# Performance work log

Hardware: AMD Instinct MI355X
Metric: run time of the kernel (lower is better)

## Reference

```python
import jax, jax.numpy as jnp
import numpy as np

MAX_DEPTH = 11  # node positions < 2**11 = 2048


def setup_inputs() -> dict:
    key = jax.random.key(0)
    k1, k2, k3, k4, k5 = jax.random.split(key, 5)
    B, S, dim = 4, 1024, 64
    token_types = jax.random.randint(k1, (B, S), 0, 5).astype(jnp.int32)
    # token_values in [-1, 2]: -1 marks out-of-scope for scope tokens;
    # bop uses tv+1 (0..3), nop uses tv+5 (4..7) -- all in-range for the 11-row table
    token_values = (jax.random.randint(k2, (B, S), 0, 4) - 1).astype(jnp.int32)
    node_positions = jax.random.randint(k3, (B, S), 0, 2048).astype(jnp.int32)
    embed_table = jax.random.normal(k4, (11, dim), dtype=jnp.float32)
    # mirrors torch.rand(2,dim,dim).softmax(-1).cumsum(-1) init
    primitives_raw = jnp.cumsum(
        jax.nn.softmax(jax.random.uniform(k5, (2, dim, dim), dtype=jnp.float32), axis=-1),
        axis=-1)
    return {
        "token_types": token_types,
        "token_values": token_values,
        "node_positions": node_positions,
        "embed_table": embed_table,
        "primitives_raw": primitives_raw,
    }


def _forward(token_types, token_values, node_positions, embed_table, primitives_raw):
    dim = embed_table.shape[1]
    B, S = token_types.shape

    # primitives = expm(P - P^H) for each of the 2 generators
    herm = primitives_raw - jnp.swapaxes(primitives_raw, -1, -2)
    prims = jax.vmap(jax.scipy.linalg.expm)(herm)  # [2, dim, dim]

    # --- positional encodings via binary-path matrix products ---
    # path(pos) applies prims[pos%2], then prims[(pos//2)%2], ... until pos==1.
    # Equivalent to the original's per-unique-position masked-linear loop,
    # evaluated per token (== positional_encodings[inverse]).
    maps = jnp.broadcast_to(jnp.eye(dim, dtype=embed_table.dtype), (B, S, dim, dim))
    pos = node_positions
    for _ in range(MAX_DEPTH):
        active = pos > 1
        bit = (pos & 1).astype(jnp.int32)
        step_p = prims[bit]  # [B, S, dim, dim] gather of the per-step generator
        # linear(maps, prim) == maps @ prim.T, applied rowwise to each map matrix
        stepped = jnp.einsum('bsij,bskj->bsik', maps, step_p)
        maps = jnp.where(active[..., None, None], stepped, maps)
        pos = pos >> 1

    # --- content embeddings via masked gathers ---
    tt, tv = token_types, token_values
    sos = tt == 0
    bop = tt == 1
    nop = tt == 2
    scope = tt == 3
    oos = scope & (tv == -1)
    db = tt == 4
    idx = jnp.where(sos, 0,
          jnp.where(bop, tv + 1,
          jnp.where(nop, tv + 5,
          jnp.where(db, 8,
          jnp.where(oos, 10, 0)))))
    valid = sos | bop | nop | db | oos  # in-scope scope tokens stay zero
    content = jnp.where(valid[..., None], embed_table[idx], jnp.zeros((), embed_table.dtype))
    return content, maps


def reference(token_types, token_values, node_positions, embed_table, primitives_raw):
    return _forward(token_types, token_values, node_positions, embed_table, primitives_raw)
```

## Files before the change

kernel.cpp:

```cpp
#include <hip/hip_runtime.h>
#include <hip/hip_bf16.h>
#include <stdint.h>

typedef __attribute__((ext_vector_type(4))) float fx4;
typedef __attribute__((ext_vector_type(16))) float fx16;
typedef __attribute__((ext_vector_type(8))) short bx8;
typedef unsigned short u16;
typedef unsigned int u32;

#define LDW 72
#define PL (64 * LDW)
#define MAGIC 0x9E3779B9u


__device__ __forceinline__ u16 f2bf(float x) {
    u32 u = __float_as_uint(x);
    return (u16)((u + 0x7FFFu + ((u >> 16) & 1u)) >> 16);
}
__device__ __forceinline__ float bf2f(u16 h) { return __uint_as_float(((u32)h) << 16); }

__device__ __forceinline__ bx8 ld32(const u16* p, int band, int kc, int l) {
    return *(const bx8*)(p + (band * 32 + (l & 31)) * LDW + kc * 16 + (l >> 5) * 8);
}

__device__ __forceinline__ void mmS(const u16* z1h, const u16* z1l,
                                    const u16* z2h, const u16* z2l,
                                    int ti, int tj, int l, fx16& acc) {
    fx16 chh, chl, clh;
#pragma unroll
    for (int i = 0; i < 16; ++i) { chh[i] = 0.f; chl[i] = 0.f; clh[i] = 0.f; }
#pragma unroll
    for (int kc = 0; kc < 4; ++kc) {
        bx8 ah = ld32(z1h, ti, kc, l), al = ld32(z1l, ti, kc, l);
        bx8 bh = ld32(z2h, tj, kc, l), bl = ld32(z2l, tj, kc, l);
        chh = __builtin_amdgcn_mfma_f32_32x32x16_bf16(ah, bh, chh, 0, 0, 0);
        chl = __builtin_amdgcn_mfma_f32_32x32x16_bf16(ah, bl, chl, 0, 0, 0);
        clh = __builtin_amdgcn_mfma_f32_32x32x16_bf16(al, bh, clh, 0, 0, 0);
    }
#pragma unroll
    for (int i = 0; i < 16; ++i) acc[i] = chh[i] + (chl[i] + clh[i]);
}

__device__ __forceinline__ void mmD(const u16* z1h, const u16* z1l,
                                    const u16* z2h, const u16* z2l,
                                    int ti, int tj, int l, fx16& a1, fx16& a2) {
    fx16 c1a, c1b, c1c, c2a, c2b, c2c;
#pragma unroll
    for (int i = 0; i < 16; ++i) {
        c1a[i] = 0.f; c1b[i] = 0.f; c1c[i] = 0.f;
        c2a[i] = 0.f; c2b[i] = 0.f; c2c[i] = 0.f;
    }
#pragma unroll
    for (int kc = 0; kc < 4; ++kc) {
        bx8 ah = ld32(z1h, ti, kc, l), al = ld32(z1l, ti, kc, l);
        bx8 bh = ld32(z2h, tj, kc, l), bl = ld32(z2l, tj, kc, l);
        c1a = __builtin_amdgcn_mfma_f32_32x32x16_bf16(ah, bh, c1a, 0, 0, 0);
        c1b = __builtin_amdgcn_mfma_f32_32x32x16_bf16(ah, bl, c1b, 0, 0, 0);
        c1c = __builtin_amdgcn_mfma_f32_32x32x16_bf16(al, bh, c1c, 0, 0, 0);
        c2a = __builtin_amdgcn_mfma_f32_32x32x16_bf16(bh, ah, c2a, 0, 0, 0);
        c2b = __builtin_amdgcn_mfma_f32_32x32x16_bf16(bh, al, c2b, 0, 0, 0);
        c2c = __builtin_amdgcn_mfma_f32_32x32x16_bf16(bl, ah, c2c, 0, 0, 0);
    }
#pragma unroll
    for (int i = 0; i < 16; ++i) {
        a1[i] = c1a[i] + (c1b[i] + c1c[i]);
        a2[i] = c2a[i] + (c2b[i] + c2c[i]);
    }
}

__device__ __forceinline__ void stP(u16* hi, u16* lo, int TI, int TJ, int l, const fx16& a) {
    const int Ar = TJ * 32 + (l & 31);
    const int c0 = TI * 32 + 4 * (l >> 5);
#pragma unroll
    for (int q = 0; q < 4; ++q) {
        union { u16 u[4]; uint2 v; } H, L;
#pragma unroll
        for (int r = 0; r < 4; ++r) {
            float v = a[4 * q + r];
            u32 u = __float_as_uint(v);
            H.u[r] = (u16)(u >> 16);
            L.u[r] = f2bf(v - __uint_as_float(u & 0xFFFF0000u));
        }
        *(uint2*)(hi + Ar * LDW + c0 + q * 8) = H.v;
        *(uint2*)(lo + Ar * LDW + c0 + q * 8) = L.v;
    }
}

__device__ __forceinline__ void stG(u16* T, int TI, int TJ, int l, const fx16& a) {
    const int Ar = TJ * 32 + (l & 31);
    const int c0 = TI * 32 + 4 * (l >> 5);
#pragma unroll
    for (int q = 0; q < 4; ++q) {
        union { u16 u[4]; uint2 v; } pk;
#pragma unroll
        for (int r = 0; r < 4; ++r) pk.u[r] = f2bf(a[4 * q + r]);
        *(uint2*)(T + Ar * 64 + c0 + q * 8) = pk.v;
    }
}

__device__ __forceinline__ void epiT32(fx16& a, const float* Mf,
                                       int TI, int TJ, int l, float qa, float qb) {
    const int gc = TJ * 32 + (l & 31);
    const int r0 = TI * 32 + 4 * (l >> 5);
#pragma unroll
    for (int q = 0; q < 4; ++q)
#pragma unroll
        for (int r = 0; r < 4; ++r) {
            const int gr = r0 + q * 8 + r;
            float m = Mf[gc * 65 + gr];
            a[4 * q + r] += qb * m + (gr == gc ? qa : 0.f);
        }
}
__device__ __forceinline__ void epiN32(fx16& a, const float* Mf,
                                       int TI, int TJ, int l, float qa, float qb) {
    const int gc = TJ * 32 + (l & 31);
    const int r0 = TI * 32 + 4 * (l >> 5);
#pragma unroll
    for (int q = 0; q < 4; ++q)
#pragma unroll
        for (int r = 0; r < 4; ++r) {
            const int gr = r0 + q * 8 + r;
            float m = Mf[gr * 65 + gc];
            a[4 * q + r] += qb * m + (gr == gc ? qa : 0.f);
        }
}

__global__ __launch_bounds__(256) void tables_kernel(const float* __restrict__ praw,
                                                     u16* __restrict__ wsP,
                                                     u16* __restrict__ rm_bf,
                                                     u16* __restrict__ cm_bf,
                                                     u32* __restrict__ flags)
{
    __shared__ u16 S[8 * PL];
    __shared__ float Mf[64 * 65];
    const int p = blockIdx.x, tid = threadIdx.x;
    const int w = tid >> 6, l = tid & 63;
    const int ti = w & 1, tj = w >> 1;

    if (p < 2) {
        const int g = p;
        const float* P = praw + g * 4096;
        u16* p0h = S;            u16* p0l = S + PL;
        u16* p1h = S + 2 * PL;   u16* p1l = S + 3 * PL;
        u16* p2h = S + 4 * PL;   u16* p2l = S + 5 * PL;
        u16* p3h = S + 6 * PL;   u16* p3l = S + 7 * PL;

        for (int s = tid; s < 4096; s += 256) {
            const int r = s >> 6, c = s & 63;
            const float m = (P[r * 64 + c] - P[c * 64 + r]) * 0.03125f;
            Mf[r * 65 + c] = m;
            u32 um = __float_as_uint(m);
            float lof = m - __uint_as_float(um & 0xFFFF0000u);
            u16 hh = (u16)(um >> 16), ll = f2bf(lof);
            p0h[r * LDW + c] = hh;  p0l[r * LDW + c] = ll;
            p1h[c * LDW + r] = hh;  p1l[c * LDW + r] = ll;
        }
        __syncthreads();

        fx16 acc, a1, a2;

        mmS(p1h, p1l, p0h, p0l, ti, tj, l, acc);
        stP(p2h, p2l, ti, tj, l, acc);
        {
            const float C8 = 2.48015873015873e-5f, C9 = 2.75573192239859e-6f;
            for (int s = tid; s < 4096; s += 256) {
                const int r = s >> 6, c = s & 63;
                float v = C9 * Mf[r * 65 + c] + (r == c ? C8 : 0.f);
                u32 u = __float_as_uint(v);
                p3h[r * LDW + c] = (u16)(u >> 16);
                p3l[r * LDW + c] = f2bf(v - __uint_as_float(u & 0xFFFF0000u));
            }
        }
        __syncthreads();

        mmS(p2h, p2l, p3h, p3l, ti, tj, l, acc);
        epiT32(acc, Mf, ti, tj, l, 1.388888888888889e-3f, 1.984126984126984e-4f);
        stP(p0h, p0l, ti, tj, l, acc);
        __syncthreads();
        mmS(p2h, p2l, p0h, p0l, ti, tj, l, acc);
        epiT32(acc, Mf, ti, tj, l, 4.166666666666667e-2f, 8.333333333333333e-3f);
        stP(p3h, p3l, ti, tj, l, acc);
        __syncthreads();
        mmS(p2h, p2l, p3h, p3l, ti, tj, l, acc);
        epiT32(acc, Mf, ti, tj, l, 0.5f, 1.666666666666667e-1f);
        stP(p0h, p0l, ti, tj, l, acc);
        __syncthreads();
        mmD(p2h, p2l, p0h, p0l, ti, tj, l, a1, a2);
        epiT32(a1, Mf, ti, tj, l, 1.f, 1.f);
        epiN32(a2, Mf, tj, ti, l, 1.f, 1.f);
        stP(p3h, p3l, ti, tj, l, a1);
        stP(p1h, p1l, tj, ti, l, a2);
        __syncthreads();

        u16 *Ych = p1h, *Ycl = p1l, *Xch = p3h, *Xcl = p3l;
        u16 *Ynh = p2h, *Ynl = p2l, *Xnh = p0h, *Xnl = p0l;
#pragma unroll 1
        for (int s5 = 0; s5 < 5; ++s5) {
            mmD(Ych, Ycl, Xch, Xcl, ti, tj, l, a1, a2);
            stP(Xnh, Xnl, ti, tj, l, a1);
            stP(Ynh, Ynl, tj, ti, l, a2);
            __syncthreads();
            u16* t;
            t = Xch; Xch = Xnh; Xnh = t;   t = Xcl; Xcl = Xnl; Xnl = t;
            t = Ych; Ych = Ynh; Ynh = t;   t = Ycl; Ycl = Ynl; Ynl = t;
        }

        for (int s8 = tid; s8 < 512; s8 += 256) {
            const int base = s8 * 8, r = base >> 6, c = base & 63;
            u16* dst = wsP + g * 16384;
            *(uint4*)(dst + base)         = *(const uint4*)(Ych + r * LDW + c);
            *(uint4*)(dst + 4096 + base)  = *(const uint4*)(Ycl + r * LDW + c);
            *(uint4*)(dst + 8192 + base)  = *(const uint4*)(Xch + r * LDW + c);
            *(uint4*)(dst + 12288 + base) = *(const uint4*)(Xcl + r * LDW + c);
        }
        __threadfence();
        __syncthreads();
        if (tid < 64) atomicExch(&flags[(g * 64 + tid) * 32], MAGIC);

        for (int s = tid; s < 4096; s += 256) {
            u16 v = ((s >> 6) == (s & 63)) ? (u16)0x3F80 : (u16)0;
            rm_bf[p * 4096 + s] = v;
            cm_bf[p * 4096 + s] = v;
        }
        return;
    }

    if (tid == 0) {
        while (atomicOr(&flags[(0 * 64 + p) * 32], 0u) != MAGIC) __builtin_amdgcn_s_sleep(8);
        while (atomicOr(&flags[(1 * 64 + p) * 32], 0u) != MAGIC) __builtin_amdgcn_s_sleep(8);
    }
    __syncthreads();
    __threadfence();

    const int d = 31 - __clz(p);

    if (d == 1) {
        const u16* src = wsP + (p & 1) * 16384;
        for (int s = tid; s < 4096; s += 256) {
            rm_bf[p * 4096 + s] = f2bf(bf2f(src[s]) + bf2f(src[4096 + s]));
            cm_bf[p * 4096 + s] = f2bf(bf2f(src[8192 + s]) + bf2f(src[12288 + s]));
        }
        return;
    }

    u16* TAh = S;            u16* TAl = S + PL;
    u16* TBh = S + 2 * PL;   u16* TBl = S + 3 * PL;
    u16* Eah = S + 4 * PL;   u16* Eal = S + 5 * PL;
    u16* Ebh = S + 6 * PL;   u16* Ebl = S + 7 * PL;

    {
        const int b0 = p & 1;
        for (int s8 = tid; s8 < 512; s8 += 256) {
            const int base = s8 * 8, r = base >> 6, c = base & 63;
            *(uint4*)(TAh + r * LDW + c) = *(const uint4*)(wsP + 8192 + base);
            *(uint4*)(TAl + r * LDW + c) = *(const uint4*)(wsP + 12288 + base);
            *(uint4*)(TBh + r * LDW + c) = *(const uint4*)(wsP + 16384 + 8192 + base);
            *(uint4*)(TBl + r * LDW + c) = *(const uint4*)(wsP + 16384 + 12288 + base);
            *(uint4*)(Eah + r * LDW + c) = *(const uint4*)(wsP + b0 * 16384 + base);
            *(uint4*)(Eal + r * LDW + c) = *(const uint4*)(wsP + b0 * 16384 + 4096 + base);
        }
    }
    __syncthreads();

    fx16 acc, a1, a2;
    u16 *Ech = Eah, *Ecl = Eal, *Enh = Ebh, *Enl = Ebl;
#pragma unroll 1
    for (int j = 1; j <= d - 2; ++j) {
        const int b = (p >> j) & 1;
        mmS(b ? TBh : TAh, b ? TBl : TAl, Ech, Ecl, ti, tj, l, acc);
        stP(Enh, Enl, ti, tj, l, acc);
        __syncthreads();
        u16* t;
        t = Ech; Ech = Enh; Enh = t;   t = Ecl; Ecl = Enl; Enl = t;
    }
    {
        const int b = (p >> (d - 1)) & 1;
        mmD(b ? TBh : TAh, b ? TBl : TAl, Ech, Ecl, ti, tj, l, a1, a2);
        stG(rm_bf + p * 4096, ti, tj, l, a1);
        stG(cm_bf + p * 4096, tj, ti, l, a2);
    }
}

__global__ __launch_bounds__(256) void out_kernel(const int* __restrict__ tt,
                                                  const int* __restrict__ tv,
                                                  const int* __restrict__ npos,
                                                  const float* __restrict__ embed,
                                                  const u16* __restrict__ rm_bf,
                                                  const u16* __restrict__ cm_bf,
                                                  float* __restrict__ out)
{
    __shared__ float ST[4][16 * 64];
    const int tid = threadIdx.x;
    const int wv = tid >> 6, l = tid & 63;
    const int flat = blockIdx.x * 4 + wv;
    const int pos = npos[flat];

    {
        const int t = tt[flat], v = tv[flat];
        int idx; bool valid = true;
        if (t == 0)      idx = 0;
        else if (t == 1) idx = v + 1;
        else if (t == 2) idx = v + 5;
        else if (t == 4) idx = 8;
        else if (t == 3 && v == -1) idx = 10;
        else { idx = 0; valid = false; }
        out[flat * 64 + l] = valid ? embed[idx * 64 + l] : 0.f;
    }

    float* om = out + 4096 * 64 + (size_t)flat * 4096;

    if (pos < 64) {
        const u16* src = rm_bf + pos * 4096;
#pragma unroll
        for (int i = 0; i < 16; ++i) {
            const int f0 = i * 256 + l * 4;
            uint2 ld = *(const uint2*)(src + f0);
            fx4 v;
            v[0] = __uint_as_float(ld.x << 16); v[1] = __uint_as_float(ld.x & 0xFFFF0000u);
            v[2] = __uint_as_float(ld.y << 16); v[3] = __uint_as_float(ld.y & 0xFFFF0000u);
            *(fx4*)(om + f0) = v;
        }
    } else {
        const int lo5 = (pos & 31) | 32;
        const int hi5 = pos >> 5;
        const u16* Acm = cm_bf + hi5 * 4096;
        const u16* Brm = rm_bf + lo5 * 4096;
        const int lr = l & 15, h = l >> 4, k8 = h * 8;
        float* st = ST[wv];

        bx8 A0[4], A1[4], B0[4], B1[4];
#pragma unroll
        for (int q = 0; q < 4; ++q) {
            A0[q] = *(const bx8*)(Acm + (q * 16 + lr) * 64 + k8);
            A1[q] = *(const bx8*)(Acm + (q * 16 + lr) * 64 + 32 + k8);
        }
#pragma unroll
        for (int c = 0; c < 4; ++c) {
            B0[c] = *(const bx8*)(Brm + (c * 16 + lr) * 64 + k8);
            B1[c] = *(const bx8*)(Brm + (c * 16 + lr) * 64 + 32 + k8);
        }
#pragma unroll
        for (int ct = 0; ct < 4; ++ct) {
#pragma unroll
            for (int q = 0; q < 4; ++q) {
                fx4 c4 = { 0.f, 0.f, 0.f, 0.f };
                c4 = __builtin_amdgcn_mfma_f32_16x16x32_bf16(A0[q], B0[ct], c4, 0, 0, 0);
                c4 = __builtin_amdgcn_mfma_f32_16x16x32_bf16(A1[q], B1[ct], c4, 0, 0, 0);
                *(fx4*)(st + lr * 64 + 4 * ((4 * q + h) ^ lr)) = c4;
            }
#pragma unroll
            for (int i2 = 0; i2 < 4; ++i2) {
                const int row = i2 * 4 + h;
                fx4 v = *(const fx4*)(st + row * 64 + 4 * ((l & 15) ^ row));
                *(fx4*)(om + ct * 1024 + i2 * 256 + l * 4) = v;
            }
        }
    }
}

extern "C" void kernel_launch(void* const* d_in, const int* in_sizes, int n_in,
                              void* d_out, int out_size, void* d_ws, size_t ws_size,
                              hipStream_t stream)
{
    const int*   tt    = (const int*)d_in[0];
    const int*   tv    = (const int*)d_in[1];
    const int*   np    = (const int*)d_in[2];
    const float* embed = (const float*)d_in[3];
    const float* praw  = (const float*)d_in[4];
    float* out = (float*)d_out;

    u32* flags = (u32*)d_ws;
    u16* wsP   = (u16*)((char*)d_ws + 16384);
    u16* rm_bf = (u16*)((char*)d_ws + 16384 + 65536);
    u16* cm_bf = (u16*)((char*)d_ws + 16384 + 65536 + 524288);

    tables_kernel<<<dim3(64), dim3(256), 0, stream>>>(praw, wsP, rm_bf, cm_bf, flags);
    out_kernel<<<dim3(1024), dim3(256), 0, stream>>>(tt, tv, np, embed, rm_bf, cm_bf, out);
}
```

Before: 40.05 us.

## Split tables kernel matmuls across two wave groups and use tree-product path tables

Doubles the tables kernel block to 512 threads so the paired row/column matmuls that used to run serially in one wave group now run concurrently in two halves. The expm scaling changes from 1/32 to 1/16, which cuts one squaring step. The path-table stage replaces its serial chain of up to d-1 matmuls with a balanced pairwise product of precomputed per-level tables, shortening the dependency chain. The cost is more LDS (14 planes), lower occupancy, and possibly slightly different accuracy from the coarser scaling.

After: 38.38 us. 4.2% less time.

```diff
diff --git a/kernel.cpp b/kernel.cpp
--- a/kernel.cpp
+++ b/kernel.cpp
@@ -23,49 +23,40 @@
     return *(const bx8*)(p + (band * 32 + (l & 31)) * LDW + kc * 16 + (l >> 5) * 8);
 }
 
-__device__ __forceinline__ void mmS(const u16* z1h, const u16* z1l,
-                                    const u16* z2h, const u16* z2l,
-                                    int ti, int tj, int l, fx16& acc) {
-    fx16 chh, chl, clh;
-#pragma unroll
-    for (int i = 0; i < 16; ++i) { chh[i] = 0.f; chl[i] = 0.f; clh[i] = 0.f; }
+__device__ __forceinline__ void mmG1(const u16* z1h, const u16* z1l,
+                                     const u16* z2h, const u16* z2l,
+                                     int ti, int tj, int l, fx16& acc) {
+    fx16 ca, cb, cc;
+#pragma unroll
+    for (int i = 0; i < 16; ++i) { ca[i] = 0.f; cb[i] = 0.f; cc[i] = 0.f; }
 #pragma unroll
     for (int kc = 0; kc < 4; ++kc) {
         bx8 ah = ld32(z1h, ti, kc, l), al = ld32(z1l, ti, kc, l);
         bx8 bh = ld32(z2h, tj, kc, l), bl = ld32(z2l, tj, kc, l);
-        chh = __builtin_amdgcn_mfma_f32_32x32x16_bf16(ah, bh, chh, 0, 0, 0);
-        chl = __builtin_amdgcn_mfma_f32_32x32x16_bf16(ah, bl, chl, 0, 0, 0);
-        clh = __builtin_amdgcn_mfma_f32_32x32x16_bf16(al, bh, clh, 0, 0, 0);
-    }
-#pragma unroll
-    for (int i = 0; i < 16; ++i) acc[i] = chh[i] + (chl[i] + clh[i]);
-}
-
-__device__ __forceinline__ void mmD(const u16* z1h, const u16* z1l,
-                                    const u16* z2h, const u16* z2l,
-                                    int ti, int tj, int l, fx16& a1, fx16& a2) {
-    fx16 c1a, c1b, c1c, c2a, c2b, c2c;
-#pragma unroll
-    for (int i = 0; i < 16; ++i) {
-        c1a[i] = 0.f; c1b[i] = 0.f; c1c[i] = 0.f;
-        c2a[i] = 0.f; c2b[i] = 0.f; c2c[i] = 0.f;
-    }
+        ca = __builtin_amdgcn_mfma_f32_32x32x16_bf16(ah, bh, ca, 0, 0, 0);
+        cb = __builtin_amdgcn_mfma_f32_32x32x16_bf16(ah, bl, cb, 0, 0, 0);
+        cc = __builtin_amdgcn_mfma_f32_32x32x16_bf16(al, bh, cc, 0, 0, 0);
+    }
+#pragma unroll
+    for (int i = 0; i < 16; ++i) acc[i] = ca[i] + (cb[i] + cc[i]);
+}
+
+__device__ __forceinline__ void mmG2(const u16* z1h, const u16* z1l,
+                                     const u16* z2h, const u16* z2l,
+                                     int ti, int tj, int l, fx16& acc) {
+    fx16 ca, cb, cc;
+#pragma unroll
+    for (int i = 0; i < 16; ++i) { ca[i] = 0.f; cb[i] = 0.f; cc[i] = 0.f; }
 #pragma unroll
     for (int kc = 0; kc < 4; ++kc) {
         bx8 ah = ld32(z1h, ti, kc, l), al = ld32(z1l, ti, kc, l);
         bx8 bh = ld32(z2h, tj, kc, l), bl = ld32(z2l, tj, kc, l);
-        c1a = __builtin_amdgcn_mfma_f32_32x32x16_bf16(ah, bh, c1a, 0, 0, 0);
-        c1b = __builtin_amdgcn_mfma_f32_32x32x16_bf16(ah, bl, c1b, 0, 0, 0);
-        c1c = __builtin_amdgcn_mfma_f32_32x32x16_bf16(al, bh, c1c, 0, 0, 0);
-        c2a = __builtin_amdgcn_mfma_f32_32x32x16_bf16(bh, ah, c2a, 0, 0, 0);
-        c2b = __builtin_amdgcn_mfma_f32_32x32x16_bf16(bh, al, c2b, 0, 0, 0);
-        c2c = __builtin_amdgcn_mfma_f32_32x32x16_bf16(bl, ah, c2c, 0, 0, 0);
-    }
-#pragma unroll
-    for (int i = 0; i < 16; ++i) {
-        a1[i] = c1a[i] + (c1b[i] + c1c[i]);
-        a2[i] = c2a[i] + (c2b[i] + c2c[i]);
-    }
+        ca = __builtin_amdgcn_mfma_f32_32x32x16_bf16(bh, ah, ca, 0, 0, 0);
+        cb = __builtin_amdgcn_mfma_f32_32x32x16_bf16(bh, al, cb, 0, 0, 0);
+        cc = __builtin_amdgcn_mfma_f32_32x32x16_bf16(bl, ah, cc, 0, 0, 0);
+    }
+#pragma unroll
+    for (int i = 0; i < 16; ++i) acc[i] = ca[i] + (cb[i] + cc[i]);
 }
 
 __device__ __forceinline__ void stP(u16* hi, u16* lo, int TI, int TJ, int l, const fx16& a) {
@@ -125,17 +116,18 @@
         }
 }
 
-__global__ __launch_bounds__(256) void tables_kernel(const float* __restrict__ praw,
+__global__ __launch_bounds__(512) void tables_kernel(const float* __restrict__ praw,
                                                      u16* __restrict__ wsP,
                                                      u16* __restrict__ rm_bf,
                                                      u16* __restrict__ cm_bf,
                                                      u32* __restrict__ flags)
 {
-    __shared__ u16 S[8 * PL];
+    __shared__ u16 S[14 * PL];
     __shared__ float Mf[64 * 65];
     const int p = blockIdx.x, tid = threadIdx.x;
     const int w = tid >> 6, l = tid & 63;
-    const int ti = w & 1, tj = w >> 1;
+    const int wid = w & 3, half = w >> 2;
+    const int ti = wid & 1, tj = wid >> 1;
 
     if (p < 2) {
         const int g = p;
@@ -145,9 +137,9 @@
         u16* p2h = S + 4 * PL;   u16* p2l = S + 5 * PL;
         u16* p3h = S + 6 * PL;   u16* p3l = S + 7 * PL;
 
-        for (int s = tid; s < 4096; s += 256) {
+        for (int s = tid; s < 4096; s += 512) {
             const int r = s >> 6, c = s & 63;
-            const float m = (P[r * 64 + c] - P[c * 64 + r]) * 0.03125f;
+            const float m = (P[r * 64 + c] - P[c * 64 + r]) * 0.0625f;
             Mf[r * 65 + c] = m;
             u32 um = __float_as_uint(m);
             float lof = m - __uint_as_float(um & 0xFFFF0000u);
@@ -157,13 +149,14 @@
         }
         __syncthreads();
 
-        fx16 acc, a1, a2;
-
-        mmS(p1h, p1l, p0h, p0l, ti, tj, l, acc);
-        stP(p2h, p2l, ti, tj, l, acc);
-        {
+        fx16 acc;
+
+        if (half == 0) {
+            mmG1(p1h, p1l, p0h, p0l, ti, tj, l, acc);
+            stP(p2h, p2l, ti, tj, l, acc);
+        } else {
             const float C8 = 2.48015873015873e-5f, C9 = 2.75573192239859e-6f;
-            for (int s = tid; s < 4096; s += 256) {
+            for (int s = tid - 256; s < 4096; s += 256) {
                 const int r = s >> 6, c = s & 63;
                 float v = C9 * Mf[r * 65 + c] + (r == c ? C8 : 0.f);
                 u32 u = __float_as_uint(v);
@@ -173,40 +166,54 @@
         }
         __syncthreads();
 
-        mmS(p2h, p2l, p3h, p3l, ti, tj, l, acc);
-        epiT32(acc, Mf, ti, tj, l, 1.388888888888889e-3f, 1.984126984126984e-4f);
-        stP(p0h, p0l, ti, tj, l, acc);
-        __syncthreads();
-        mmS(p2h, p2l, p0h, p0l, ti, tj, l, acc);
-        epiT32(acc, Mf, ti, tj, l, 4.166666666666667e-2f, 8.333333333333333e-3f);
-        stP(p3h, p3l, ti, tj, l, acc);
-        __syncthreads();
-        mmS(p2h, p2l, p3h, p3l, ti, tj, l, acc);
-        epiT32(acc, Mf, ti, tj, l, 0.5f, 1.666666666666667e-1f);
-        stP(p0h, p0l, ti, tj, l, acc);
-        __syncthreads();
-        mmD(p2h, p2l, p0h, p0l, ti, tj, l, a1, a2);
-        epiT32(a1, Mf, ti, tj, l, 1.f, 1.f);
-        epiN32(a2, Mf, tj, ti, l, 1.f, 1.f);
-        stP(p3h, p3l, ti, tj, l, a1);
-        stP(p1h, p1l, tj, ti, l, a2);
+        if (half == 0) {
+            mmG1(p2h, p2l, p3h, p3l, ti, tj, l, acc);
+            epiT32(acc, Mf, ti, tj, l, 1.388888888888889e-3f, 1.984126984126984e-4f);
+            stP(p0h, p0l, ti, tj, l, acc);
+        }
+        __syncthreads();
+        if (half == 0) {
+            mmG1(p2h, p2l, p0h, p0l, ti, tj, l, acc);
+            epiT32(acc, Mf, ti, tj, l, 4.166666666666667e-2f, 8.333333333333333e-3f);
+            stP(p3h, p3l, ti, tj, l, acc);
+        }
+        __syncthreads();
+        if (half == 0) {
+            mmG1(p2h, p2l, p3h, p3l, ti, tj, l, acc);
+            epiT32(acc, Mf, ti, tj, l, 0.5f, 1.666666666666667e-1f);
+            stP(p0h, p0l, ti, tj, l, acc);
+        }
+        __syncthreads();
+        if (half == 0) {
+            mmG1(p2h, p2l, p0h, p0l, ti, tj, l, acc);
+            epiT32(acc, Mf, ti, tj, l, 1.f, 1.f);
+            stP(p3h, p3l, ti, tj, l, acc);
+        } else {
+            mmG2(p2h, p2l, p0h, p0l, ti, tj, l, acc);
+            epiN32(acc, Mf, tj, ti, l, 1.f, 1.f);
+            stP(p1h, p1l, tj, ti, l, acc);
+        }
         __syncthreads();
 
         u16 *Ych = p1h, *Ycl = p1l, *Xch = p3h, *Xcl = p3l;
         u16 *Ynh = p2h, *Ynl = p2l, *Xnh = p0h, *Xnl = p0l;
 #pragma unroll 1
-        for (int s5 = 0; s5 < 5; ++s5) {
-            mmD(Ych, Ycl, Xch, Xcl, ti, tj, l, a1, a2);
-            stP(Xnh, Xnl, ti, tj, l, a1);
-            stP(Ynh, Ynl, tj, ti, l, a2);
+        for (int s4 = 0; s4 < 4; ++s4) {
+            if (half == 0) {
+                mmG1(Ych, Ycl, Xch, Xcl, ti, tj, l, acc);
+                stP(Xnh, Xnl, ti, tj, l, acc);
+            } else {
+                mmG2(Ych, Ycl, Xch, Xcl, ti, tj, l, acc);
+                stP(Ynh, Ynl, tj, ti, l, acc);
+            }
             __syncthreads();
             u16* t;
             t = Xch; Xch = Xnh; Xnh = t;   t = Xcl; Xcl = Xnl; Xnl = t;
             t = Ych; Ych = Ynh; Ynh = t;   t = Ycl; Ycl = Ynl; Ynl = t;
         }
 
-        for (int s8 = tid; s8 < 512; s8 += 256) {
-            const int base = s8 * 8, r = base >> 6, c = base & 63;
+        {
+            const int base = tid * 8, r = base >> 6, c = base & 63;
             u16* dst = wsP + g * 16384;
             *(uint4*)(dst + base)         = *(const uint4*)(Ych + r * LDW + c);
             *(uint4*)(dst + 4096 + base)  = *(const uint4*)(Ycl + r * LDW + c);
@@ -217,7 +224,7 @@
         __syncthreads();
         if (tid < 64) atomicExch(&flags[(g * 64 + tid) * 32], MAGIC);
 
-        for (int s = tid; s < 4096; s += 256) {
+        for (int s = tid; s < 4096; s += 512) {
             u16 v = ((s >> 6) == (s & 63)) ? (u16)0x3F80 : (u16)0;
             rm_bf[p * 4096 + s] = v;
             cm_bf[p * 4096 + s] = v;
@@ -236,48 +243,78 @@
 
     if (d == 1) {
         const u16* src = wsP + (p & 1) * 16384;
-        for (int s = tid; s < 4096; s += 256) {
+        for (int s = tid; s < 4096; s += 512) {
             rm_bf[p * 4096 + s] = f2bf(bf2f(src[s]) + bf2f(src[4096 + s]));
             cm_bf[p * 4096 + s] = f2bf(bf2f(src[8192 + s]) + bf2f(src[12288 + s]));
         }
         return;
     }
 
-    u16* TAh = S;            u16* TAl = S + PL;
-    u16* TBh = S + 2 * PL;   u16* TBl = S + 3 * PL;
-    u16* Eah = S + 4 * PL;   u16* Eal = S + 5 * PL;
-    u16* Ebh = S + 6 * PL;   u16* Ebl = S + 7 * PL;
-
     {
-        const int b0 = p & 1;
-        for (int s8 = tid; s8 < 512; s8 += 256) {
-            const int base = s8 * 8, r = base >> 6, c = base & 63;
-            *(uint4*)(TAh + r * LDW + c) = *(const uint4*)(wsP + 8192 + base);
-            *(uint4*)(TAl + r * LDW + c) = *(const uint4*)(wsP + 12288 + base);
-            *(uint4*)(TBh + r * LDW + c) = *(const uint4*)(wsP + 16384 + 8192 + base);
-            *(uint4*)(TBl + r * LDW + c) = *(const uint4*)(wsP + 16384 + 12288 + base);
-            *(uint4*)(Eah + r * LDW + c) = *(const uint4*)(wsP + b0 * 16384 + base);
-            *(uint4*)(Eal + r * LDW + c) = *(const uint4*)(wsP + b0 * 16384 + 4096 + base);
-        }
+        const int base = tid * 8, r = base >> 6, c = base & 63;
+        const int off = r * LDW + c;
+        *(uint4*)(S + 0 * PL + off) = *(const uint4*)(wsP + base);
+        *(uint4*)(S + 1 * PL + off) = *(const uint4*)(wsP + 4096 + base);
+        *(uint4*)(S + 2 * PL + off) = *(const uint4*)(wsP + 8192 + base);
+        *(uint4*)(S + 3 * PL + off) = *(const uint4*)(wsP + 12288 + base);
+        *(uint4*)(S + 4 * PL + off) = *(const uint4*)(wsP + 16384 + base);
+        *(uint4*)(S + 5 * PL + off) = *(const uint4*)(wsP + 16384 + 4096 + base);
+        *(uint4*)(S + 6 * PL + off) = *(const uint4*)(wsP + 16384 + 8192 + base);
+        *(uint4*)(S + 7 * PL + off) = *(const uint4*)(wsP + 16384 + 12288 + base);
     }
     __syncthreads();
 
-    fx16 acc, a1, a2;
-    u16 *Ech = Eah, *Ecl = Eal, *Enh = Ebh, *Enl = Ebl;
-#pragma unroll 1
-    for (int j = 1; j <= d - 2; ++j) {
-        const int b = (p >> j) & 1;
-        mmS(b ? TBh : TAh, b ? TBl : TAl, Ech, Ecl, ti, tj, l, acc);
-        stP(Enh, Enl, ti, tj, l, acc);
-        __syncthreads();
-        u16* t;
-        t = Ech; Ech = Enh; Enh = t;   t = Ecl; Ecl = Enl; Enl = t;
-    }
-    {
-        const int b = (p >> (d - 1)) & 1;
-        mmD(b ? TBh : TAh, b ? TBl : TAl, Ech, Ecl, ti, tj, l, a1, a2);
-        stG(rm_bf + p * 4096, ti, tj, l, a1);
-        stG(cm_bf + p * 4096, tj, ti, l, a2);
+    const int b0 = p & 1, b1 = (p >> 1) & 1, b2 = (p >> 2) & 1, b3 = (p >> 3) & 1,
+              b4 = (p >> 4) & 1;
+    const u16 *rm0h = S + b0 * 4 * PL,          *rm0l = rm0h + PL;
+    const u16 *cm1h = S + b1 * 4 * PL + 2 * PL, *cm1l = cm1h + PL;
+    const u16 *rm2h = S + b2 * 4 * PL,          *rm2l = rm2h + PL;
+    const u16 *cm3h = S + b3 * 4 * PL + 2 * PL, *cm3l = cm3h + PL;
+    u16 *PAh = S + 8 * PL,  *PAl = S + 9 * PL;
+    u16 *PBh = S + 10 * PL, *PBl = S + 11 * PL;
+    u16 *PCh = S + 12 * PL, *PCl = S + 13 * PL;
+
+    fx16 acc;
+    const u16 *fz1h, *fz1l, *fz2h, *fz2l;
+
+    if (d == 2) {
+        fz1h = cm1h; fz1l = cm1l; fz2h = rm0h; fz2l = rm0l;
+    } else if (d == 3) {
+        if (half == 0) {
+            mmG1(cm1h, cm1l, rm0h, rm0l, ti, tj, l, acc);
+            stP(PAh, PAl, ti, tj, l, acc);
+        }
+        __syncthreads();
+        const u16* c2h = S + b2 * 4 * PL + 2 * PL;
+        fz1h = c2h; fz1l = c2h + PL; fz2h = PAh; fz2l = PAl;
+    } else {
+        if (half == 0) {
+            mmG1(cm1h, cm1l, rm0h, rm0l, ti, tj, l, acc);
+            stP(PAh, PAl, ti, tj, l, acc);
+        } else {
+            mmG2(cm3h, cm3l, rm2h, rm2l, ti, tj, l, acc);
+            stP(PBh, PBl, tj, ti, l, acc);
+        }
+        __syncthreads();
+        if (d == 4) {
+            fz1h = PBh; fz1l = PBl; fz2h = PAh; fz2l = PAl;
+        } else {
+            if (half == 0) {
+                mmG1(PBh, PBl, PAh, PAl, ti, tj, l, acc);
+                stP(PCh, PCl, ti, tj, l, acc);
+            }
+            __syncthreads();
+            const u16* c4h = S + b4 * 4 * PL + 2 * PL;
+            fz1h = c4h; fz1l = c4h + PL; fz2h = PCh; fz2l = PCl;
+        }
+    }
+
+    if (half == 0) {
+        mmG1(fz1h, fz1l, fz2h, fz2l, ti, tj, l, acc);
+        stG(rm_bf + p * 4096, ti, tj, l, acc);
+    } else {
+        mmG2(fz1h, fz1l, fz2h, fz2l, ti, tj, l, acc);
+        stG(cm_bf + p * 4096, tj, ti, l, acc);
     }
 }
 
@@ -374,6 +411,6 @@
     u16* rm_bf = (u16*)((char*)d_ws + 16384 + 65536);
     u16* cm_bf = (u16*)((char*)d_ws + 16384 + 65536 + 524288);
 
-    tables_kernel<<<dim3(64), dim3(256), 0, stream>>>(praw, wsP, rm_bf, cm_bf, flags);
+    tables_kernel<<<dim3(64), dim3(512), 0, stream>>>(praw, wsP, rm_bf, cm_bf, flags);
     out_kernel<<<dim3(1024), dim3(256), 0, stream>>>(tt, tv, np, embed, rm_bf, cm_bf, out);
 }
```
